# Performance work log

Hardware: AMD Instinct MI355X
Metric: run time of the kernel (lower is better)

Reference implementation:

```python
import jax, jax.numpy as jnp
import numpy as np

INPUT_SIZE = 10000
GROUP_SIZE = 500
STEP = GROUP_SIZE // 2            # 250
OUT_PER_GROUP = 50
GROUPS = 2 * INPUT_SIZE // GROUP_SIZE - 1  # 39


def setup_inputs() -> dict:
    key = jax.random.key(0)
    k1, k2 = jax.random.split(key)
    x = jax.random.uniform(k1, (4096, INPUT_SIZE), dtype=jnp.float32)
    # torch init: uniform_(weight, 0.9, 1.1); weight shape per group is [out, in]
    W = jax.random.uniform(k2, (GROUPS, OUT_PER_GROUP, GROUP_SIZE),
                           dtype=jnp.float32, minval=0.9, maxval=1.1)
    return {"x": x, "W": W}


def reference(x, W):
    # gather overlapping windows: idx[g, k] = g*STEP + k  -> [B, GROUPS, GROUP_SIZE]
    idx = jnp.arange(GROUPS)[:, None] * STEP + jnp.arange(GROUP_SIZE)[None, :]
    xw = x[:, idx]                                   # [B, G, K]
    # per-group linear (no bias): out[b,g,o] = sum_k xw[b,g,k] * W[g,o,k]
    out = jnp.einsum('bgk,gok->bgo', xw, W)          # [B, G, O]
    return jax.nn.relu(out.reshape(x.shape[0], GROUPS * OUT_PER_GROUP))
```

## Files before the change

kernel.cpp:

```cpp
#include <hip/hip_runtime.h>
#include <hip/hip_bf16.h>


constexpr int INPUT  = 10000;
constexpr int GROUPS = 39;
constexpr int GS     = 500;
constexpr int STEP   = 250;
constexpr int OPG    = 50;
constexpr int OUTW   = 1950;
constexpr int KP     = 512;
constexpr int BM     = 32;
constexpr int LDA    = KP + 8;

__device__ __hip_bfloat16 Wb[GROUPS * OPG * KP];

typedef __attribute__((ext_vector_type(8))) short  short8;
typedef __attribute__((ext_vector_type(4))) float  float4v;

__device__ __forceinline__ unsigned bf2pack(float a, float b) {
    union { float f; unsigned u; } x, y; x.f = a; y.f = b;
    unsigned lo = (x.u + 0x7fffu + ((x.u >> 16) & 1u)) >> 16;
    unsigned hi = (y.u + 0x7fffu + ((y.u >> 16) & 1u)) & 0xffff0000u;
    return hi | lo;
}

__global__ void prep_w(const float* __restrict__ W) {
    const int slot = blockIdx.x * 256 + threadIdx.x;
    if (slot >= GROUPS * OPG * (KP / 2)) return;
    const int go = slot / (KP / 2);
    const int k  = (slot - go * (KP / 2)) * 2;
    float2 v = {0.f, 0.f};
    if (k < GS) v = *(const float2*)(W + (size_t)go * GS + k);
    ((unsigned*)Wb)[slot] = bf2pack(v.x, v.y);
}

__global__ __launch_bounds__(256, 4)
void peak_binner_kernel(const float* __restrict__ x,
                        float* __restrict__ out, int batch)
{
    __shared__ __align__(16) short As[BM * LDA];

    const int g    = blockIdx.x;
    const int m0   = blockIdx.y * BM;
    const int tid  = threadIdx.x;
    const int lane = tid & 63;
    const int wave = tid >> 6;
    const int fm   = lane & 15;
    const int l4   = lane >> 4;
    const int nb   = (wave == 3) ? 34 : wave * 16;

    const bool lvalid = (tid < STEP);
    #pragma unroll
    for (int bb = 0; bb < 4; ++bb) {
        float2 v[8];
        #pragma unroll
        for (int j = 0; j < 8; ++j) {
            const int it = bb * 8 + j;
            const int gr = min(m0 + it, batch - 1);
            v[j] = lvalid ? *(const float2*)(x + (size_t)gr * INPUT + g * STEP + 2 * tid)
                          : float2{0.f, 0.f};
        }
        #pragma unroll
        for (int j = 0; j < 8; ++j) {
            const int it = bb * 8 + j;
            *(unsigned*)&As[it * LDA + 2 * tid] = bf2pack(v[j].x, v[j].y);
        }
    }

    float4v acc[2] = {{0,0,0,0},{0,0,0,0}};
    const __hip_bfloat16* wp = Wb + ((size_t)g * OPG + nb + fm) * KP + l4 * 8;

    __syncthreads();

    #pragma unroll
    for (int kk = 0; kk < 16; ++kk) {
        const short8 b  = *(const short8*)(wp + kk * 32);
        const short8 a0 = *(const short8*)&As[fm        * LDA + kk * 32 + l4 * 8];
        const short8 a1 = *(const short8*)&As[(16 + fm) * LDA + kk * 32 + l4 * 8];
        acc[0] = __builtin_amdgcn_mfma_f32_16x16x32_bf16(a0, b, acc[0], 0, 0, 0);
        acc[1] = __builtin_amdgcn_mfma_f32_16x16x32_bf16(a1, b, acc[1], 0, 0, 0);
    }

    if (wave < 3 || fm >= 14) {
        const int col = g * OPG + nb + fm;
        #pragma unroll
        for (int mt = 0; mt < 2; ++mt)
            #pragma unroll
            for (int reg = 0; reg < 4; ++reg) {
                const int row = m0 + mt * 16 + l4 * 4 + reg;
                if (row < batch)
                    out[(size_t)row * OUTW + col] = fmaxf(acc[mt][reg], 0.f);
            }
    }
}

extern "C" void kernel_launch(void* const* d_in, const int* in_sizes, int n_in,
                              void* d_out, int out_size, void* d_ws, size_t ws_size,
                              hipStream_t stream) {
    const float* x = (const float*)d_in[0];
    const float* W = (const float*)d_in[1];
    float* out     = (float*)d_out;

    const int batch = in_sizes[0] / INPUT;

    const int slots = GROUPS * OPG * (KP / 2);
    prep_w<<<(slots + 255) / 256, 256, 0, stream>>>(W);

    dim3 grid(GROUPS, (batch + BM - 1) / BM);
    peak_binner_kernel<<<grid, dim3(256), 0, stream>>>(x, out, batch);
}
```

Baseline: 280.7 us.

## Stream x tile directly into LDS as fp32 and prefetch weight fragments

New measurement: 275.8 us. About the same (-1.7%).

```diff
diff --git a/kernel.cpp b/kernel.cpp
--- a/kernel.cpp
+++ b/kernel.cpp
@@ -10,7 +10,7 @@
 constexpr int OUTW   = 1950;
 constexpr int KP     = 512;
 constexpr int BM     = 32;
-constexpr int LDA    = KP + 8;
+constexpr int LDAF   = 516;
 
 __device__ __hip_bfloat16 Wb[GROUPS * OPG * KP];
 
@@ -34,11 +34,11 @@
     ((unsigned*)Wb)[slot] = bf2pack(v.x, v.y);
 }
 
-__global__ __launch_bounds__(256, 4)
+__global__ __launch_bounds__(256, 2)
 void peak_binner_kernel(const float* __restrict__ x,
                         float* __restrict__ out, int batch)
 {
-    __shared__ __align__(16) short As[BM * LDA];
+    __shared__ __align__(16) float As[BM * LDAF];
 
     const int g    = blockIdx.x;
     const int m0   = blockIdx.y * BM;
@@ -49,36 +49,62 @@
     const int l4   = lane >> 4;
     const int nb   = (wave == 3) ? 34 : wave * 16;
 
-    const bool lvalid = (tid < STEP);
+    const __hip_bfloat16* wp = Wb + ((size_t)g * OPG + nb + fm) * KP + l4 * 8;
+    short8 bfrag[16];
     #pragma unroll
-    for (int bb = 0; bb < 4; ++bb) {
-        float2 v[8];
+    for (int j = 0; j < 16; ++j)
+        bfrag[j] = *(const short8*)(wp + j * 32);
+
+    if (tid < 96) {
+        const int r = tid / 3, c = 500 + (tid % 3) * 4;
+        *(float4v*)&As[r * LDAF + c] = float4v{0.f, 0.f, 0.f, 0.f};
+    }
+
+    {
+        const int r0 = wave * 8;
         #pragma unroll
         for (int j = 0; j < 8; ++j) {
-            const int it = bb * 8 + j;
-            const int gr = min(m0 + it, batch - 1);
-            v[j] = lvalid ? *(const float2*)(x + (size_t)gr * INPUT + g * STEP + 2 * tid)
-                          : float2{0.f, 0.f};
-        }
-        #pragma unroll
-        for (int j = 0; j < 8; ++j) {
-            const int it = bb * 8 + j;
-            *(unsigned*)&As[it * LDA + 2 * tid] = bf2pack(v[j].x, v[j].y);
+            const int r  = r0 + j;
+            const int gr = min(m0 + r, batch - 1);
+            const float* src = x + (size_t)gr * INPUT + g * STEP;
+            __builtin_amdgcn_global_load_lds(
+                (const __attribute__((address_space(1))) void*)(src + lane * 4),
+                (__attribute__((address_space(3))) void*)&As[r * LDAF],
+                16, 0, 0);
+            if (lane < 61)
+                __builtin_amdgcn_global_load_lds(
+                    (const __attribute__((address_space(1))) void*)(src + 256 + lane * 4),
+                    (__attribute__((address_space(3))) void*)&As[r * LDAF + 256],
+                    16, 0, 0);
         }
     }
 
+    #pragma unroll
+    for (int j = 0; j < 16; ++j)
+        asm volatile("" :: "v"(bfrag[j]));
+
     float4v acc[2] = {{0,0,0,0},{0,0,0,0}};
-    const __hip_bfloat16* wp = Wb + ((size_t)g * OPG + nb + fm) * KP + l4 * 8;
 
     __syncthreads();
 
     #pragma unroll
     for (int kk = 0; kk < 16; ++kk) {
-        const short8 b  = *(const short8*)(wp + kk * 32);
-        const short8 a0 = *(const short8*)&As[fm        * LDA + kk * 32 + l4 * 8];
-        const short8 a1 = *(const short8*)&As[(16 + fm) * LDA + kk * 32 + l4 * 8];
-        acc[0] = __builtin_amdgcn_mfma_f32_16x16x32_bf16(a0, b, acc[0], 0, 0, 0);
-        acc[1] = __builtin_amdgcn_mfma_f32_16x16x32_bf16(a1, b, acc[1], 0, 0, 0);
+        const int cb = kk * 32 + l4 * 8;
+        const float4v f0 = *(const float4v*)&As[fm        * LDAF + cb];
+        const float4v f1 = *(const float4v*)&As[fm        * LDAF + cb + 4];
+        const float4v h0 = *(const float4v*)&As[(16 + fm) * LDAF + cb];
+        const float4v h1 = *(const float4v*)&As[(16 + fm) * LDAF + cb + 4];
+        short8 a0, a1;
+        ((unsigned*)&a0)[0] = bf2pack(f0[0], f0[1]);
+        ((unsigned*)&a0)[1] = bf2pack(f0[2], f0[3]);
+        ((unsigned*)&a0)[2] = bf2pack(f1[0], f1[1]);
+        ((unsigned*)&a0)[3] = bf2pack(f1[2], f1[3]);
+        ((unsigned*)&a1)[0] = bf2pack(h0[0], h0[1]);
+        ((unsigned*)&a1)[1] = bf2pack(h0[2], h0[3]);
+        ((unsigned*)&a1)[2] = bf2pack(h1[0], h1[1]);
+        ((unsigned*)&a1)[3] = bf2pack(h1[2], h1[3]);
+        acc[0] = __builtin_amdgcn_mfma_f32_16x16x32_bf16(a0, bfrag[kk], acc[0], 0, 0, 0);
+        acc[1] = __builtin_amdgcn_mfma_f32_16x16x32_bf16(a1, bfrag[kk], acc[1], 0, 0, 0);
     }
 
     if (wave < 3 || fm >= 14) {
```

## Make GEMM blocks persistent with double-buffered async global-to-LDS loads

Applied to the files above, without the earlier changes.

Measured after the change: 258.3 us. -8.0%, faster.

```diff
diff --git a/kernel.cpp b/kernel.cpp
--- a/kernel.cpp
+++ b/kernel.cpp
@@ -9,13 +9,17 @@
 constexpr int OPG    = 50;
 constexpr int OUTW   = 1950;
 constexpr int KP     = 512;
-constexpr int BM     = 32;
-constexpr int LDA    = KP + 8;
+constexpr int BMT    = 16;
+constexpr int LDAF   = 516;
+constexpr int NBY    = 13;
 
 __device__ __hip_bfloat16 Wb[GROUPS * OPG * KP];
 
 typedef __attribute__((ext_vector_type(8))) short  short8;
 typedef __attribute__((ext_vector_type(4))) float  float4v;
+
+#define GPTR const __attribute__((address_space(1))) void*
+#define LPTR __attribute__((address_space(3))) void*
 
 __device__ __forceinline__ unsigned bf2pack(float a, float b) {
     union { float f; unsigned u; } x, y; x.f = a; y.f = b;
@@ -34,14 +38,14 @@
     ((unsigned*)Wb)[slot] = bf2pack(v.x, v.y);
 }
 
-__global__ __launch_bounds__(256, 4)
+__global__ __launch_bounds__(256, 2)
 void peak_binner_kernel(const float* __restrict__ x,
                         float* __restrict__ out, int batch)
 {
-    __shared__ __align__(16) short As[BM * LDA];
+    __shared__ __align__(16) float As[2][BMT * LDAF];
 
     const int g    = blockIdx.x;
-    const int m0   = blockIdx.y * BM;
+    const int by   = blockIdx.y;
     const int tid  = threadIdx.x;
     const int lane = tid & 63;
     const int wave = tid >> 6;
@@ -49,48 +53,91 @@
     const int l4   = lane >> 4;
     const int nb   = (wave == 3) ? 34 : wave * 16;
 
-    const bool lvalid = (tid < STEP);
+    const int mt = batch >> 4;
+    const int T  = (mt - by + NBY - 1) / NBY;
+
+    const __hip_bfloat16* wp = Wb + ((size_t)g * OPG + nb + fm) * KP + l4 * 8;
+    short8 bfrag[16];
     #pragma unroll
-    for (int bb = 0; bb < 4; ++bb) {
-        float2 v[8];
-        #pragma unroll
-        for (int j = 0; j < 8; ++j) {
-            const int it = bb * 8 + j;
-            const int gr = min(m0 + it, batch - 1);
-            v[j] = lvalid ? *(const float2*)(x + (size_t)gr * INPUT + g * STEP + 2 * tid)
-                          : float2{0.f, 0.f};
-        }
-        #pragma unroll
-        for (int j = 0; j < 8; ++j) {
-            const int it = bb * 8 + j;
-            *(unsigned*)&As[it * LDA + 2 * tid] = bf2pack(v[j].x, v[j].y);
-        }
+    for (int j = 0; j < 16; ++j)
+        bfrag[j] = *(const short8*)(wp + j * 32);
+
+    if (tid < 128) {
+        const int r = tid >> 2;
+        const int c = 500 + (tid & 3) * 4;
+        *(float4v*)&((&As[0][0])[r * LDAF + c]) = float4v{0.f, 0.f, 0.f, 0.f};
     }
 
-    float4v acc[2] = {{0,0,0,0},{0,0,0,0}};
-    const __hip_bfloat16* wp = Wb + ((size_t)g * OPG + nb + fm) * KP + l4 * 8;
+    auto STAGE = [&](int t, int pb) {
+        const int my = by + NBY * t;
+        const int r0 = wave * 4;
+        #pragma unroll
+        for (int j = 0; j < 4; ++j) {
+            const int r = r0 + j;
+            const float* src = x + (size_t)(my * BMT + r) * INPUT + g * STEP;
+            __builtin_amdgcn_global_load_lds((GPTR)(src + lane * 4),
+                                             (LPTR)&As[pb][r * LDAF], 16, 0, 0);
+            if (lane < 61)
+                __builtin_amdgcn_global_load_lds((GPTR)(src + 256 + lane * 4),
+                                                 (LPTR)&As[pb][r * LDAF + 256], 16, 0, 0);
+        }
+    };
 
-    __syncthreads();
+    float4v acc;
+    auto COMPUTE = [&](int pb) {
+        acc = float4v{0.f, 0.f, 0.f, 0.f};
+        const float* Ab = &As[pb][0];
+        #pragma unroll
+        for (int kk = 0; kk < 16; ++kk) {
+            const int cb = kk * 32 + l4 * 8;
+            const float4v f0 = *(const float4v*)&Ab[fm * LDAF + cb];
+            const float4v f1 = *(const float4v*)&Ab[fm * LDAF + cb + 4];
+            short8 a;
+            ((unsigned*)&a)[0] = bf2pack(f0[0], f0[1]);
+            ((unsigned*)&a)[1] = bf2pack(f0[2], f0[3]);
+            ((unsigned*)&a)[2] = bf2pack(f1[0], f1[1]);
+            ((unsigned*)&a)[3] = bf2pack(f1[2], f1[3]);
+            acc = __builtin_amdgcn_mfma_f32_16x16x32_bf16(a, bfrag[kk], acc, 0, 0, 0);
+        }
+    };
 
-    #pragma unroll
-    for (int kk = 0; kk < 16; ++kk) {
-        const short8 b  = *(const short8*)(wp + kk * 32);
-        const short8 a0 = *(const short8*)&As[fm        * LDA + kk * 32 + l4 * 8];
-        const short8 a1 = *(const short8*)&As[(16 + fm) * LDA + kk * 32 + l4 * 8];
-        acc[0] = __builtin_amdgcn_mfma_f32_16x16x32_bf16(a0, b, acc[0], 0, 0, 0);
-        acc[1] = __builtin_amdgcn_mfma_f32_16x16x32_bf16(a1, b, acc[1], 0, 0, 0);
-    }
-
-    if (wave < 3 || fm >= 14) {
-        const int col = g * OPG + nb + fm;
-        #pragma unroll
-        for (int mt = 0; mt < 2; ++mt)
+    auto EPI = [&](int t) {
+        if (wave < 3 || fm >= 14) {
+            const int col = g * OPG + nb + fm;
+            const int my  = by + NBY * t;
             #pragma unroll
             for (int reg = 0; reg < 4; ++reg) {
-                const int row = m0 + mt * 16 + l4 * 4 + reg;
-                if (row < batch)
-                    out[(size_t)row * OUTW + col] = fmaxf(acc[mt][reg], 0.f);
+                const int row = my * BMT + l4 * 4 + reg;
+                out[(size_t)row * OUTW + col] = fmaxf(acc[reg], 0.f);
             }
+        }
+    };
+
+    STAGE(0, 0);
+    if (T > 1) STAGE(1, 1);
+    asm volatile("s_waitcnt vmcnt(8) lgkmcnt(0)" ::: "memory");
+    __builtin_amdgcn_sched_barrier(0);
+    __builtin_amdgcn_s_barrier();
+    __builtin_amdgcn_sched_barrier(0);
+    COMPUTE(0);
+    EPI(0);
+    __builtin_amdgcn_s_barrier();
+    __builtin_amdgcn_sched_barrier(0);
+
+    for (int t = 1; t < T; ++t) {
+        if (t + 1 < T) {
+            STAGE(t + 1, (t + 1) & 1);
+            asm volatile("s_waitcnt vmcnt(12)" ::: "memory");
+        } else {
+            asm volatile("s_waitcnt vmcnt(4)" ::: "memory");
+        }
+        __builtin_amdgcn_sched_barrier(0);
+        __builtin_amdgcn_s_barrier();
+        __builtin_amdgcn_sched_barrier(0);
+        COMPUTE(t & 1);
+        EPI(t);
+        __builtin_amdgcn_s_barrier();
+        __builtin_amdgcn_sched_barrier(0);
     }
 }
 
@@ -106,6 +153,6 @@
     const int slots = GROUPS * OPG * (KP / 2);
     prep_w<<<(slots + 255) / 256, 256, 0, stream>>>(W);
 
-    dim3 grid(GROUPS, (batch + BM - 1) / BM);
+    dim3 grid(GROUPS, NBY);
     peak_binner_kernel<<<grid, dim3(256), 0, stream>>>(x, out, batch);
 }
```

## Make GEMM blocks persistent with register-resident B and double-buffered A loads

Applied to the files above, without the earlier changes.

Result: faster. 255.7 us (-8.9%).

```diff
diff --git a/kernel.cpp b/kernel.cpp
--- a/kernel.cpp
+++ b/kernel.cpp
@@ -9,13 +9,26 @@
 constexpr int OPG    = 50;
 constexpr int OUTW   = 1950;
 constexpr int KP     = 512;
-constexpr int BM     = 32;
-constexpr int LDA    = KP + 8;
+constexpr int BMT    = 16;
+constexpr int LDA16  = 520;
+constexpr int NBY    = 19;
 
 __device__ __hip_bfloat16 Wb[GROUPS * OPG * KP];
 
 typedef __attribute__((ext_vector_type(8))) short  short8;
 typedef __attribute__((ext_vector_type(4))) float  float4v;
+
+#define WAITV(n) do { \
+    asm volatile("s_waitcnt vmcnt(" #n ")" ::: "memory"); \
+    __builtin_amdgcn_sched_barrier(0); \
+} while (0)
+
+#define LGKM_BAR() do { \
+    asm volatile("s_waitcnt lgkmcnt(0)" ::: "memory"); \
+    __builtin_amdgcn_sched_barrier(0); \
+    __builtin_amdgcn_s_barrier(); \
+    __builtin_amdgcn_sched_barrier(0); \
+} while (0)
 
 __device__ __forceinline__ unsigned bf2pack(float a, float b) {
     union { float f; unsigned u; } x, y; x.f = a; y.f = b;
@@ -34,14 +47,14 @@
     ((unsigned*)Wb)[slot] = bf2pack(v.x, v.y);
 }
 
-__global__ __launch_bounds__(256, 4)
+__global__ __launch_bounds__(256, 3)
 void peak_binner_kernel(const float* __restrict__ x,
                         float* __restrict__ out, int batch)
 {
-    __shared__ __align__(16) short As[BM * LDA];
+    __shared__ __align__(16) short As[2][BMT * LDA16];
 
     const int g    = blockIdx.x;
-    const int m0   = blockIdx.y * BM;
+    const int by   = blockIdx.y;
     const int tid  = threadIdx.x;
     const int lane = tid & 63;
     const int wave = tid >> 6;
@@ -49,48 +62,87 @@
     const int l4   = lane >> 4;
     const int nb   = (wave == 3) ? 34 : wave * 16;
 
-    const bool lvalid = (tid < STEP);
+    const int mt = batch >> 4;
+    const int T  = (mt - by + NBY - 1) / NBY;
+
+    const __hip_bfloat16* wp = Wb + ((size_t)g * OPG + nb + fm) * KP + l4 * 8;
+    short8 bfrag[16];
     #pragma unroll
-    for (int bb = 0; bb < 4; ++bb) {
-        float2 v[8];
+    for (int j = 0; j < 16; ++j)
+        bfrag[j] = *(const short8*)(wp + j * 32);
+
+    const bool ld0 = (lane <= 62), ld1 = (lane <= 61);
+    const float* xbase = x + (size_t)g * STEP + 8 * lane;
+
+    auto ISSUE = [&](int t, float4v* v) {
+        const float* b0 = xbase + (size_t)((by + NBY * t) * BMT + wave * 4) * INPUT;
         #pragma unroll
-        for (int j = 0; j < 8; ++j) {
-            const int it = bb * 8 + j;
-            const int gr = min(m0 + it, batch - 1);
-            v[j] = lvalid ? *(const float2*)(x + (size_t)gr * INPUT + g * STEP + 2 * tid)
-                          : float2{0.f, 0.f};
+        for (int j = 0; j < 4; ++j) {
+            const float* src = b0 + (size_t)j * INPUT;
+            v[2*j]   = ld0 ? *(const float4v*)(src)     : float4v{0,0,0,0};
+            v[2*j+1] = ld1 ? *(const float4v*)(src + 4) : float4v{0,0,0,0};
         }
+    };
+
+    auto CONVERT = [&](const float4v* v, int pb) {
         #pragma unroll
-        for (int j = 0; j < 8; ++j) {
-            const int it = bb * 8 + j;
-            *(unsigned*)&As[it * LDA + 2 * tid] = bf2pack(v[j].x, v[j].y);
+        for (int j = 0; j < 4; ++j) {
+            const int r = wave * 4 + j;
+            short8 w;
+            ((unsigned*)&w)[0] = bf2pack(v[2*j][0],   v[2*j][1]);
+            ((unsigned*)&w)[1] = bf2pack(v[2*j][2],   v[2*j][3]);
+            ((unsigned*)&w)[2] = bf2pack(v[2*j+1][0], v[2*j+1][1]);
+            ((unsigned*)&w)[3] = bf2pack(v[2*j+1][2], v[2*j+1][3]);
+            *(short8*)&As[pb][r * LDA16 + 8 * lane] = w;
         }
-    }
+    };
 
-    float4v acc[2] = {{0,0,0,0},{0,0,0,0}};
-    const __hip_bfloat16* wp = Wb + ((size_t)g * OPG + nb + fm) * KP + l4 * 8;
+    float4v acc;
+    auto COMPUTE = [&](int pb) {
+        acc = float4v{0.f, 0.f, 0.f, 0.f};
+        __builtin_amdgcn_s_setprio(1);
+        #pragma unroll
+        for (int kk = 0; kk < 16; ++kk) {
+            const short8 a = *(const short8*)&As[pb][fm * LDA16 + kk * 32 + l4 * 8];
+            acc = __builtin_amdgcn_mfma_f32_16x16x32_bf16(a, bfrag[kk], acc, 0, 0, 0);
+        }
+        __builtin_amdgcn_s_setprio(0);
+    };
 
-    __syncthreads();
+    auto EPI = [&](int t) {
+        if (wave < 3 || fm >= 14) {
+            const int col = g * OPG + nb + fm;
+            const int my  = by + NBY * t;
+            #pragma unroll
+            for (int reg = 0; reg < 4; ++reg)
+                out[(size_t)(my * BMT + l4 * 4 + reg) * OUTW + col] = fmaxf(acc[reg], 0.f);
+        }
+    };
 
-    #pragma unroll
-    for (int kk = 0; kk < 16; ++kk) {
-        const short8 b  = *(const short8*)(wp + kk * 32);
-        const short8 a0 = *(const short8*)&As[fm        * LDA + kk * 32 + l4 * 8];
-        const short8 a1 = *(const short8*)&As[(16 + fm) * LDA + kk * 32 + l4 * 8];
-        acc[0] = __builtin_amdgcn_mfma_f32_16x16x32_bf16(a0, b, acc[0], 0, 0, 0);
-        acc[1] = __builtin_amdgcn_mfma_f32_16x16x32_bf16(a1, b, acc[1], 0, 0, 0);
-    }
+    float4v vA[8], vB[8];
 
-    if (wave < 3 || fm >= 14) {
-        const int col = g * OPG + nb + fm;
-        #pragma unroll
-        for (int mt = 0; mt < 2; ++mt)
-            #pragma unroll
-            for (int reg = 0; reg < 4; ++reg) {
-                const int row = m0 + mt * 16 + l4 * 4 + reg;
-                if (row < batch)
-                    out[(size_t)row * OUTW + col] = fmaxf(acc[mt][reg], 0.f);
-            }
+    ISSUE(0, vA);
+    ISSUE(1, vB);
+    WAITV(8);
+    CONVERT(vA, 0);
+    LGKM_BAR();
+
+    for (int t = 0; ; t += 2) {
+        const bool n2 = (t + 2 < T);
+        if (n2) ISSUE(t + 2, vA);
+        COMPUTE(0); EPI(t);
+        if (t + 1 >= T) break;
+        if (n2) { if (t == 0) WAITV(12); else WAITV(16); } else WAITV(8);
+        CONVERT(vB, 1);
+        LGKM_BAR();
+
+        const bool n3 = (t + 3 < T);
+        if (n3) ISSUE(t + 3, vB);
+        COMPUTE(1); EPI(t + 1);
+        if (!n2) break;
+        if (n3) WAITV(16); else WAITV(8);
+        CONVERT(vA, 0);
+        LGKM_BAR();
     }
 }
 
@@ -106,6 +158,6 @@
     const int slots = GROUPS * OPG * (KP / 2);
     prep_w<<<(slots + 255) / 256, 256, 0, stream>>>(W);
 
-    dim3 grid(GROUPS, (batch + BM - 1) / BM);
+    dim3 grid(GROUPS, NBY);
     peak_binner_kernel<<<grid, dim3(256), 0, stream>>>(x, out, batch);
 }
```
